# Kernel tuning notes

Measured on AMD Instinct MI355X. Metric: run time of the kernel, lower is better.

## Reference

```python
import jax, jax.numpy as jnp
import numpy as np

N = 100000      # nodes
E = 1600000     # edges (avg degree 16)
IN = 128        # input_dim
HID = 32        # hidden_dim per head (layer 1)
HEADS = 2       # heads (layer 1)
OUT = 32        # output_dim (layer 2, heads=1)
NEG_SLOPE = 0.2 # PyG GATConv default leaky relu slope


def setup_inputs() -> dict:
    key = jax.random.key(0)
    ks = jax.random.split(key, 10)
    s = 0.1  # glorot-ish scale
    x = jax.random.normal(ks[0], (N, IN), jnp.float32)
    edge_index = jax.random.randint(ks[1], (2, E), 0, N, dtype=jnp.int64)
    W1 = jax.random.normal(ks[2], (IN, HEADS * HID), jnp.float32) * s
    a1_src = jax.random.normal(ks[3], (HEADS, HID), jnp.float32) * s
    a1_dst = jax.random.normal(ks[4], (HEADS, HID), jnp.float32) * s
    b1 = jnp.zeros((HEADS * HID,), jnp.float32)
    W2 = jax.random.normal(ks[5], (HEADS * HID, OUT), jnp.float32) * s
    a2_src = jax.random.normal(ks[6], (1, OUT), jnp.float32) * s
    a2_dst = jax.random.normal(ks[7], (1, OUT), jnp.float32) * s
    b2 = jnp.zeros((OUT,), jnp.float32)
    return {"x": x, "edge_index": edge_index, "W1": W1, "a1_src": a1_src,
            "a1_dst": a1_dst, "b1": b1, "W2": W2, "a2_src": a2_src,
            "a2_dst": a2_dst, "b2": b2}


def _gat_layer(x, src, dst, W, a_src, a_dst, b, heads, out_ch, concat, n_nodes):
    # linear projection: [N, heads, out_ch]
    h = (x @ W).reshape(n_nodes, heads, out_ch)
    # per-node attention halves: [N, heads]
    alpha_s = jnp.einsum('nhc,hc->nh', h, a_src)
    alpha_d = jnp.einsum('nhc,hc->nh', h, a_dst)
    # per-edge raw score (message x_j = source node, softmax over dst segment)
    e = jax.nn.leaky_relu(alpha_s[src] + alpha_d[dst], NEG_SLOPE)  # [E, heads]
    # segment softmax over incoming edges of each dst node
    m = jax.ops.segment_max(e, dst, num_segments=n_nodes)          # [N, heads]
    m = jax.lax.stop_gradient(m)
    ee = jnp.exp(e - m[dst])
    denom = jax.ops.segment_sum(ee, dst, num_segments=n_nodes)     # [N, heads]
    alpha = ee / (denom[dst] + 1e-16)                              # [E, heads]
    # weighted scatter-add aggregation
    msg = h[src] * alpha[:, :, None]                               # [E, heads, out_ch]
    out = jax.ops.segment_sum(msg, dst, num_segments=n_nodes)      # [N, heads, out_ch]
    if concat:
        out = out.reshape(n_nodes, heads * out_ch)
    else:
        out = out.mean(axis=1)
    return out + b


def reference(x, edge_index, W1, a1_src, a1_dst, b1, W2, a2_src, a2_dst, b2):
    n = x.shape[0]
    # PyG GATConv adds self-loops by default (both layers, same edge set)
    loop = jnp.arange(n, dtype=edge_index.dtype)
    src = jnp.concatenate([edge_index[0], loop])
    dst = jnp.concatenate([edge_index[1], loop])
    h = _gat_layer(x, src, dst, W1, a1_src, a1_dst, b1, HEADS, HID, True, n)
    h = jax.nn.elu(h)
    return _gat_layer(h, src, dst, W2, a2_src, a2_dst, b2, 1, OUT, False, n)
```

## Files before the change

kernel.cpp:

```cpp
#include <hip/hip_runtime.h>
#include <math.h>

#define N_NODES 100000
#define N_EDGES 1600000
#define IN_DIM  128
#define C1      64
#define OUT_DIM 32
#define NEG_SLOPE 0.2f
#define LOG2E 1.44269504f

#define BSHIFT  8
#define BNODES  256
#define NBUCK   ((N_NODES + BNODES - 1) / BNODES)
#define CAP     5120
#define SLOTS   48
#define GC_STRIDE 16
#define G1_BLOCKS ((N_NODES + 127) / 128)

typedef _Float16 half8 __attribute__((ext_vector_type(8)));
typedef float    f32x4 __attribute__((ext_vector_type(4)));

__device__ __forceinline__ float wexp2(float sc) {
    return __builtin_amdgcn_exp2f(fmaxf(sc, NEG_SLOPE * sc));
}


__global__ void zero_k(int4* __restrict__ p, int n4) {
    int i = blockIdx.x * 256 + threadIdx.x;
    if (i < n4) p[i] = make_int4(0, 0, 0, 0);
}

__global__ __launch_bounds__(1024) void binp1_k(const int* __restrict__ ei,
        int* __restrict__ gcur, int* __restrict__ buf) {
    __shared__ int scnt[NBUCK], sbase[NBUCK], soff[NBUCK];
    int t = threadIdx.x;
    if (t < NBUCK) { scnt[t] = 0; soff[t] = 0; }
    __syncthreads();
    int  s[16], bk[16], ld[16];
    bool v[16];
    #pragma unroll
    for (int i = 0; i < 16; ++i) {
        int e = blockIdx.x * 16384 + i * 1024 + t;
        v[i] = e < N_EDGES;
        int ec = v[i] ? e : 0;
        s[i] = ei[ec];
        int d = ei[N_EDGES + ec];
        bk[i] = d >> BSHIFT;
        ld[i] = d & (BNODES - 1);
        if (v[i]) atomicAdd(&scnt[bk[i]], 1);
    }
    __syncthreads();
    if (t < NBUCK) sbase[t] = atomicAdd(&gcur[t * GC_STRIDE], scnt[t]);
    __syncthreads();
    #pragma unroll
    for (int i = 0; i < 16; ++i) {
        if (v[i]) {
            int p = sbase[bk[i]] + atomicAdd(&soff[bk[i]], 1);
            if (p < CAP) buf[bk[i] * CAP + p] = s[i] | (ld[i] << 17);
        }
    }
}

__global__ __launch_bounds__(256) void binp2_k(const int* __restrict__ gcur,
        const int* __restrict__ buf, int* __restrict__ csr, int* __restrict__ deg) {
    __shared__ int4 lcsr4[BNODES * SLOTS / 4];
    __shared__ int  lcnt[BNODES];
    int* lcsr = (int*)lcsr4;
    int b = blockIdx.x, t = threadIdx.x;
    lcnt[t] = 0;
    __syncthreads();
    int cnt = gcur[b * GC_STRIDE];
    if (cnt > CAP) cnt = CAP;
    const int* bb = buf + b * CAP;
    for (int e = t; e < cnt; e += 256) {
        int vv = bb[e];
        int src = vv & 0x1FFFF;
        int l = vv >> 17;
        int slot = atomicAdd(&lcnt[l], 1);
        if (slot < SLOTS) lcsr[l * SLOTS + slot] = src;
    }
    __syncthreads();
    int c = lcnt[t];
    int slot = c < SLOTS ? c : SLOTS - 1;
    lcsr[t * SLOTS + slot] = b * BNODES + t;
    int cd = c + 1;
    deg[b * BNODES + t] = cd < SLOTS ? cd : SLOTS;
    __syncthreads();
    int4* g4 = (int4*)csr + (size_t)b * (BNODES * SLOTS / 4);
    #pragma unroll
    for (int i = 0; i < BNODES * SLOTS / 4 / 256; ++i)
        g4[t + i * 256] = lcsr4[t + i * 256];
}

__global__ void prep_k(const float* __restrict__ W1, const float* __restrict__ W2,
                       _Float16* __restrict__ w1t, _Float16* __restrict__ w2t) {
    int t = blockIdx.x * 256 + threadIdx.x;
    if (t < IN_DIM * C1) {
        int k = t >> 6, n = t & 63;
        w1t[n * IN_DIM + k] = (_Float16)W1[t];
    }
    if (t < C1 * OUT_DIM) {
        int k = t >> 5, n = t & 31;
        w2t[n * C1 + k] = (_Float16)W2[t];
    }
}

__global__ __launch_bounds__(256) void gemm1_k(const float* __restrict__ x,
        const _Float16* __restrict__ w1t, const float* __restrict__ a_s,
        const float* __restrict__ a_d, _Float16* __restrict__ h,
        float* __restrict__ as_o, float* __restrict__ ad_o) {
    __shared__ _Float16 sh[4][32 * 72];
    int t = threadIdx.x;
    int wv = t >> 6, lane = t & 63, m = lane & 15, q = lane >> 4;
    int rbw = blockIdx.x * 128 + wv * 32;
    f32x4 acc[2][4];
    #pragma unroll
    for (int i = 0; i < 2; ++i)
        #pragma unroll
        for (int j = 0; j < 4; ++j) acc[i][j] = (f32x4){0.f, 0.f, 0.f, 0.f};
    #pragma unroll
    for (int ks = 0; ks < 4; ++ks) {
        half8 a[2];
        #pragma unroll
        for (int rt = 0; rt < 2; ++rt) {
            int r = rbw + rt * 16 + m;
            r = r < N_NODES ? r : 0;
            const float4* p = (const float4*)(x + (size_t)r * IN_DIM + ks * 32 + q * 8);
            float4 f0 = p[0], f1 = p[1];
            half8 av;
            av[0] = (_Float16)f0.x; av[1] = (_Float16)f0.y;
            av[2] = (_Float16)f0.z; av[3] = (_Float16)f0.w;
            av[4] = (_Float16)f1.x; av[5] = (_Float16)f1.y;
            av[6] = (_Float16)f1.z; av[7] = (_Float16)f1.w;
            a[rt] = av;
        }
        #pragma unroll
        for (int ct = 0; ct < 4; ++ct) {
            half8 b = *(const half8*)(w1t + (ct * 16 + m) * IN_DIM + ks * 32 + q * 8);
            acc[0][ct] = __builtin_amdgcn_mfma_f32_16x16x32_f16(a[0], b, acc[0][ct], 0, 0, 0);
            acc[1][ct] = __builtin_amdgcn_mfma_f32_16x16x32_f16(a[1], b, acc[1][ct], 0, 0, 0);
        }
    }
    _Float16* ws = sh[wv];
    #pragma unroll
    for (int rt = 0; rt < 2; ++rt)
        #pragma unroll
        for (int ct = 0; ct < 4; ++ct)
            #pragma unroll
            for (int r = 0; r < 4; ++r)
                ws[(rt * 16 + q * 4 + r) * 72 + ct * 16 + m] = (_Float16)acc[rt][ct][r];
    __syncthreads();
    int rl = lane >> 1, hp = lane & 1;
    int rg = rbw + rl;
    if (rg < N_NODES) {
        float As_r[32], Ad_r[32];
        const float4* ap = (const float4*)(a_s + hp * 32);
        const float4* dp = (const float4*)(a_d + hp * 32);
        #pragma unroll
        for (int i = 0; i < 8; ++i) {
            float4 v = ap[i];
            As_r[4*i] = v.x; As_r[4*i+1] = v.y; As_r[4*i+2] = v.z; As_r[4*i+3] = v.w;
            float4 u = dp[i];
            Ad_r[4*i] = u.x; Ad_r[4*i+1] = u.y; Ad_r[4*i+2] = u.z; Ad_r[4*i+3] = u.w;
        }
        const _Float16* rowp = ws + rl * 72 + hp * 32;
        half8 c0 = *(const half8*)(rowp);
        half8 c1 = *(const half8*)(rowp + 8);
        half8 c2 = *(const half8*)(rowp + 16);
        half8 c3 = *(const half8*)(rowp + 24);
        float s = 0.f, dd = 0.f;
        #pragma unroll
        for (int j = 0; j < 8; ++j) {
            s  = fmaf((float)c0[j], As_r[j],      s);
            dd = fmaf((float)c0[j], Ad_r[j],      dd);
            s  = fmaf((float)c1[j], As_r[8 + j],  s);
            dd = fmaf((float)c1[j], Ad_r[8 + j],  dd);
            s  = fmaf((float)c2[j], As_r[16 + j], s);
            dd = fmaf((float)c2[j], Ad_r[16 + j], dd);
            s  = fmaf((float)c3[j], As_r[24 + j], s);
            dd = fmaf((float)c3[j], Ad_r[24 + j], dd);
        }
        as_o[rg * 2 + hp] = s  * LOG2E;
        ad_o[rg * 2 + hp] = dd * LOG2E;
        _Float16* hr = h + (size_t)rg * C1 + hp * 32;
        *(half8*)(hr)      = c0;
        *(half8*)(hr + 8)  = c1;
        *(half8*)(hr + 16) = c2;
        *(half8*)(hr + 24) = c3;
    }
}

__global__ __launch_bounds__(256) void agg1g2_k(const int* __restrict__ deg,
        const int* __restrict__ csr, const _Float16* __restrict__ h1,
        const float* __restrict__ as1, const float* __restrict__ ad1,
        const float* __restrict__ b1, const _Float16* __restrict__ w2t,
        const float* __restrict__ a2s, const float* __restrict__ a2d,
        _Float16* __restrict__ h2, float* __restrict__ as2o,
        float* __restrict__ ad2o) {
    __shared__ _Float16 shu[16 * 72];
    __shared__ _Float16 sh2[16 * 36];
    int t = threadIdx.x;
    int wv = t >> 6, lane = t & 63;
    int dl   = lane >> 4;
    int eg   = (lane >> 3) & 1;
    int cl   = lane & 7;
    int head = cl >> 2;
    int lr   = wv * 4 + dl;
    int d    = blockIdx.x * 16 + lr;

    int cnt = deg[d];
    const int* row = csr + d * SLOTS;
    float advl = ad1[d * 2 + head];
    float acc[8] = {0.f, 0.f, 0.f, 0.f, 0.f, 0.f, 0.f, 0.f};
    float wsum = 0.f;
    for (int base = 0; base < cnt; base += 8) {
        int e0 = base + eg, e1 = e0 + 2, e2 = e0 + 4, e3 = e0 + 6;
        bool v0 = e0 < cnt, v1 = e1 < cnt, v2 = e2 < cnt, v3 = e3 < cnt;
        int s0 = row[v0 ? e0 : 0];
        int s1 = row[v1 ? e1 : 0];
        int s2 = row[v2 ? e2 : 0];
        int s3 = row[v3 ? e3 : 0];
        float a0 = as1[(unsigned)(s0 * 2 + head)];
        float a1 = as1[(unsigned)(s1 * 2 + head)];
        float a2 = as1[(unsigned)(s2 * 2 + head)];
        float a3 = as1[(unsigned)(s3 * 2 + head)];
        half8 g0 = *(const half8*)(h1 + (unsigned)(s0 * C1 + 8 * cl));
        half8 g1 = *(const half8*)(h1 + (unsigned)(s1 * C1 + 8 * cl));
        half8 g2 = *(const half8*)(h1 + (unsigned)(s2 * C1 + 8 * cl));
        half8 g3 = *(const half8*)(h1 + (unsigned)(s3 * C1 + 8 * cl));
        float w0 = v0 ? wexp2(a0 + advl) : 0.f;
        float w1 = v1 ? wexp2(a1 + advl) : 0.f;
        float w2 = v2 ? wexp2(a2 + advl) : 0.f;
        float w3 = v3 ? wexp2(a3 + advl) : 0.f;
        #pragma unroll
        for (int i = 0; i < 8; ++i) {
            acc[i] = fmaf((float)g0[i], w0, acc[i]);
            acc[i] = fmaf((float)g1[i], w1, acc[i]);
            acc[i] = fmaf((float)g2[i], w2, acc[i]);
            acc[i] = fmaf((float)g3[i], w3, acc[i]);
        }
        wsum += (w0 + w1) + (w2 + w3);
    }
    #pragma unroll
    for (int i = 0; i < 8; ++i) acc[i] += __shfl_xor(acc[i], 8);
    wsum += __shfl_xor(wsum, 8);
    if (eg == 0) {
        float inv = 1.f / (wsum + 1e-16f);
        const float4* bv = (const float4*)(b1 + 8 * cl);
        float o[8];
        #pragma unroll
        for (int i = 0; i < 4; ++i) {
            o[i]     = acc[i]     * inv + (&bv[0].x)[i];
            o[4 + i] = acc[4 + i] * inv + (&bv[1].x)[i];
        }
        half8 hv;
        #pragma unroll
        for (int i = 0; i < 8; ++i) {
            float e = o[i] > 0.f ? o[i] : __expf(o[i]) - 1.f;
            hv[i] = (_Float16)e;
        }
        *(half8*)(shu + lr * 72 + cl * 8) = hv;
    }
    __syncthreads();
    if (wv != 0) return;

    {
        int m = lane & 15, q = lane >> 4;
        f32x4 c2[2];
        c2[0] = (f32x4){0.f, 0.f, 0.f, 0.f};
        c2[1] = (f32x4){0.f, 0.f, 0.f, 0.f};
        #pragma unroll
        for (int ks = 0; ks < 2; ++ks) {
            half8 a = *(const half8*)(shu + m * 72 + ks * 32 + q * 8);
            #pragma unroll
            for (int ct = 0; ct < 2; ++ct) {
                half8 b = *(const half8*)(w2t + (ct * 16 + m) * C1 + ks * 32 + q * 8);
                c2[ct] = __builtin_amdgcn_mfma_f32_16x16x32_f16(a, b, c2[ct], 0, 0, 0);
            }
        }
        #pragma unroll
        for (int ct = 0; ct < 2; ++ct)
            #pragma unroll
            for (int r = 0; r < 4; ++r)
                sh2[(q * 4 + r) * 36 + ct * 16 + m] = (_Float16)c2[ct][r];
    }
    asm volatile("s_waitcnt lgkmcnt(0)" ::: "memory");

    {
        int r = lane & 15, p = lane >> 4;
        int rg = blockIdx.x * 16 + r;
        const float4* ap = (const float4*)(a2s + p * 8);
        const float4* dp = (const float4*)(a2d + p * 8);
        float4 av0 = ap[0], av1 = ap[1];
        float4 dv0 = dp[0], dv1 = dp[1];
        float As[8] = {av0.x, av0.y, av0.z, av0.w, av1.x, av1.y, av1.z, av1.w};
        float Ad[8] = {dv0.x, dv0.y, dv0.z, dv0.w, dv1.x, dv1.y, dv1.z, dv1.w};
        half8 c = *(const half8*)(sh2 + r * 36 + p * 8);
        float s = 0.f, dd = 0.f;
        #pragma unroll
        for (int j = 0; j < 8; ++j) {
            s  = fmaf((float)c[j], As[j], s);
            dd = fmaf((float)c[j], Ad[j], dd);
        }
        s  += __shfl_xor(s, 16);  s  += __shfl_xor(s, 32);
        dd += __shfl_xor(dd, 16); dd += __shfl_xor(dd, 32);
        if (p == 0) {
            as2o[rg] = s  * LOG2E;
            ad2o[rg] = dd * LOG2E;
        }
        *(half8*)(h2 + (size_t)rg * OUT_DIM + p * 8) = c;
    }
}

__global__ __launch_bounds__(256) void agg2_k(const int* __restrict__ deg,
        const int* __restrict__ csr, const _Float16* __restrict__ h2,
        const float* __restrict__ as2, const float* __restrict__ ad2,
        const float* __restrict__ b2, float* __restrict__ out) {
    int lane = threadIdx.x & 63;
    int dl   = lane >> 3;
    int eg   = (lane >> 2) & 1;
    int cl   = lane & 3;
    int d = ((blockIdx.x * 256 + threadIdx.x) >> 6) * 8 + dl;
    int cnt = deg[d];
    const int* row = csr + d * SLOTS;
    float advl = ad2[d];
    float acc[8] = {0.f, 0.f, 0.f, 0.f, 0.f, 0.f, 0.f, 0.f};
    float wsum = 0.f;
    for (int base = 0; base < cnt; base += 8) {
        int e0 = base + eg, e1 = e0 + 2, e2 = e0 + 4, e3 = e0 + 6;
        bool v0 = e0 < cnt, v1 = e1 < cnt, v2 = e2 < cnt, v3 = e3 < cnt;
        int s0 = row[v0 ? e0 : 0];
        int s1 = row[v1 ? e1 : 0];
        int s2 = row[v2 ? e2 : 0];
        int s3 = row[v3 ? e3 : 0];
        float a0 = as2[(unsigned)s0];
        float a1 = as2[(unsigned)s1];
        float a2 = as2[(unsigned)s2];
        float a3 = as2[(unsigned)s3];
        half8 g0 = *(const half8*)(h2 + (unsigned)(s0 * OUT_DIM + 8 * cl));
        half8 g1 = *(const half8*)(h2 + (unsigned)(s1 * OUT_DIM + 8 * cl));
        half8 g2 = *(const half8*)(h2 + (unsigned)(s2 * OUT_DIM + 8 * cl));
        half8 g3 = *(const half8*)(h2 + (unsigned)(s3 * OUT_DIM + 8 * cl));
        float w0 = v0 ? wexp2(a0 + advl) : 0.f;
        float w1 = v1 ? wexp2(a1 + advl) : 0.f;
        float w2 = v2 ? wexp2(a2 + advl) : 0.f;
        float w3 = v3 ? wexp2(a3 + advl) : 0.f;
        #pragma unroll
        for (int i = 0; i < 8; ++i) {
            acc[i] = fmaf((float)g0[i], w0, acc[i]);
            acc[i] = fmaf((float)g1[i], w1, acc[i]);
            acc[i] = fmaf((float)g2[i], w2, acc[i]);
            acc[i] = fmaf((float)g3[i], w3, acc[i]);
        }
        wsum += (w0 + w1) + (w2 + w3);
    }
    #pragma unroll
    for (int i = 0; i < 8; ++i) acc[i] += __shfl_xor(acc[i], 4);
    wsum += __shfl_xor(wsum, 4);
    if (eg == 0) {
        float inv = 1.f / (wsum + 1e-16f);
        const float4* bv = (const float4*)(b2 + 8 * cl);
        float4 o0, o1;
        o0.x = acc[0] * inv + bv[0].x; o0.y = acc[1] * inv + bv[0].y;
        o0.z = acc[2] * inv + bv[0].z; o0.w = acc[3] * inv + bv[0].w;
        o1.x = acc[4] * inv + bv[1].x; o1.y = acc[5] * inv + bv[1].y;
        o1.z = acc[6] * inv + bv[1].z; o1.w = acc[7] * inv + bv[1].w;
        float4* ow = (float4*)(out + (size_t)d * OUT_DIM + 8 * cl);
        ow[0] = o0;
        ow[1] = o1;
    }
}


extern "C" void kernel_launch(void* const* d_in, const int* in_sizes, int n_in,
                              void* d_out, int out_size, void* d_ws, size_t ws_size,
                              hipStream_t stream) {
    const float* x   = (const float*)d_in[0];
    const int*   ei  = (const int*)d_in[1];
    const float* W1  = (const float*)d_in[2];
    const float* a1s = (const float*)d_in[3];
    const float* a1d = (const float*)d_in[4];
    const float* b1  = (const float*)d_in[5];
    const float* W2  = (const float*)d_in[6];
    const float* a2s = (const float*)d_in[7];
    const float* a2d = (const float*)d_in[8];
    const float* b2  = (const float*)d_in[9];
    float* out = (float*)d_out;

    char* ws = (char*)d_ws;
    size_t off = 0;
    auto alloc = [&](size_t bytes) -> void* {
        void* p = ws + off;
        off = (off + bytes + 255) & ~(size_t)255;
        return p;
    };
    int* gcur      = (int*)alloc((size_t)NBUCK * GC_STRIDE * 4);
    int* buf       = (int*)alloc((size_t)NBUCK * CAP * 4);
    int* csr       = (int*)alloc((size_t)NBUCK * BNODES * SLOTS * 4);
    int* deg       = (int*)alloc((size_t)NBUCK * BNODES * 4);
    _Float16* w1t  = (_Float16*)alloc((size_t)IN_DIM * C1 * 2);
    _Float16* w2t  = (_Float16*)alloc((size_t)C1 * OUT_DIM * 2);
    _Float16* h1   = (_Float16*)alloc((size_t)N_NODES * C1 * 2);
    float* as1     = (float*)alloc((size_t)N_NODES * 2 * 4);
    float* ad1     = (float*)alloc((size_t)N_NODES * 2 * 4);
    _Float16* h2   = (_Float16*)alloc((size_t)N_NODES * OUT_DIM * 2);
    float* as2     = (float*)alloc((size_t)N_NODES * 4);
    float* ad2     = (float*)alloc((size_t)N_NODES * 4);

    const int ZN4 = NBUCK * GC_STRIDE / 4;
    zero_k<<<(ZN4 + 255) / 256, 256, 0, stream>>>((int4*)gcur, ZN4);
    binp1_k<<<(N_EDGES + 16383) / 16384, 1024, 0, stream>>>(ei, gcur, buf);
    binp2_k<<<NBUCK, 256, 0, stream>>>(gcur, buf, csr, deg);
    prep_k<<<(IN_DIM * C1 + 255) / 256, 256, 0, stream>>>(W1, W2, w1t, w2t);

    gemm1_k<<<G1_BLOCKS, 256, 0, stream>>>(x, w1t, a1s, a1d, h1, as1, ad1);
    agg1g2_k<<<N_NODES / 16, 256, 0, stream>>>(deg, csr, h1, as1, ad1, b1,
                                               w2t, a2s, a2d, h2, as2, ad2);
    agg2_k<<<N_NODES / 32, 256, 0, stream>>>(deg, csr, h2, as2, ad2, b2, out);
}
```

Before: 217.6 us.

## Fold gcur zeroing into prep, shrink binning blocks, stage CSR rows in LDS

The zeroing of the bucket counters moves into prep_k, which now runs before binning, so one kernel launch goes away. binp1 switches from 1024-thread to 256-thread blocks with four times as many blocks, and skips global atomics for buckets with a zero count. Both aggregation kernels load their block's CSR rows into shared memory with coalesced int4 reads, instead of each lane reading neighbour indices from global memory. A sched_barrier is added after the LDS wait in agg1g2. This costs more shared memory per block plus one extra __syncthreads, and binning now issues more global atomics because there are more blocks.

```diff
diff --git a/kernel.cpp b/kernel.cpp
--- a/kernel.cpp
+++ b/kernel.cpp
@@ -25,22 +25,17 @@
 }
 
 
-__global__ void zero_k(int4* __restrict__ p, int n4) {
-    int i = blockIdx.x * 256 + threadIdx.x;
-    if (i < n4) p[i] = make_int4(0, 0, 0, 0);
-}
-
-__global__ __launch_bounds__(1024) void binp1_k(const int* __restrict__ ei,
+__global__ __launch_bounds__(256) void binp1_k(const int* __restrict__ ei,
         int* __restrict__ gcur, int* __restrict__ buf) {
     __shared__ int scnt[NBUCK], sbase[NBUCK], soff[NBUCK];
     int t = threadIdx.x;
-    if (t < NBUCK) { scnt[t] = 0; soff[t] = 0; }
+    for (int i = t; i < NBUCK; i += 256) { scnt[i] = 0; soff[i] = 0; }
     __syncthreads();
     int  s[16], bk[16], ld[16];
     bool v[16];
     #pragma unroll
     for (int i = 0; i < 16; ++i) {
-        int e = blockIdx.x * 16384 + i * 1024 + t;
+        int e = blockIdx.x * 4096 + i * 256 + t;
         v[i] = e < N_EDGES;
         int ec = v[i] ? e : 0;
         s[i] = ei[ec];
@@ -50,7 +45,8 @@
         if (v[i]) atomicAdd(&scnt[bk[i]], 1);
     }
     __syncthreads();
-    if (t < NBUCK) sbase[t] = atomicAdd(&gcur[t * GC_STRIDE], scnt[t]);
+    for (int i = t; i < NBUCK; i += 256)
+        sbase[i] = scnt[i] ? atomicAdd(&gcur[i * GC_STRIDE], scnt[i]) : 0;
     __syncthreads();
     #pragma unroll
     for (int i = 0; i < 16; ++i) {
@@ -93,8 +89,10 @@
 }
 
 __global__ void prep_k(const float* __restrict__ W1, const float* __restrict__ W2,
-                       _Float16* __restrict__ w1t, _Float16* __restrict__ w2t) {
+                       _Float16* __restrict__ w1t, _Float16* __restrict__ w2t,
+                       int* __restrict__ gcur) {
     int t = blockIdx.x * 256 + threadIdx.x;
+    if (t < NBUCK * GC_STRIDE) gcur[t] = 0;
     if (t < IN_DIM * C1) {
         int k = t >> 6, n = t & 63;
         w1t[n * IN_DIM + k] = (_Float16)W1[t];
@@ -197,6 +195,7 @@
         const float* __restrict__ a2s, const float* __restrict__ a2d,
         _Float16* __restrict__ h2, float* __restrict__ as2o,
         float* __restrict__ ad2o) {
+    __shared__ int      srow[16 * SLOTS];
     __shared__ _Float16 shu[16 * 72];
     __shared__ _Float16 sh2[16 * 36];
     int t = threadIdx.x;
@@ -208,8 +207,12 @@
     int lr   = wv * 4 + dl;
     int d    = blockIdx.x * 16 + lr;
 
+    if (t < 16 * SLOTS / 4)
+        ((int4*)srow)[t] = ((const int4*)(csr + (size_t)blockIdx.x * 16 * SLOTS))[t];
+    __syncthreads();
+
     int cnt = deg[d];
-    const int* row = csr + d * SLOTS;
+    const int* row = srow + lr * SLOTS;
     float advl = ad1[d * 2 + head];
     float acc[8] = {0.f, 0.f, 0.f, 0.f, 0.f, 0.f, 0.f, 0.f};
     float wsum = 0.f;
@@ -285,6 +288,7 @@
                 sh2[(q * 4 + r) * 36 + ct * 16 + m] = (_Float16)c2[ct][r];
     }
     asm volatile("s_waitcnt lgkmcnt(0)" ::: "memory");
+    __builtin_amdgcn_sched_barrier(0);
 
     {
         int r = lane & 15, p = lane >> 4;
@@ -316,13 +320,25 @@
         const int* __restrict__ csr, const _Float16* __restrict__ h2,
         const float* __restrict__ as2, const float* __restrict__ ad2,
         const float* __restrict__ b2, float* __restrict__ out) {
-    int lane = threadIdx.x & 63;
+    __shared__ int srow[32 * SLOTS];
+    int t = threadIdx.x;
+    int wv = t >> 6, lane = t & 63;
     int dl   = lane >> 3;
     int eg   = (lane >> 2) & 1;
     int cl   = lane & 3;
-    int d = ((blockIdx.x * 256 + threadIdx.x) >> 6) * 8 + dl;
+    int lr   = wv * 8 + dl;
+    int d    = blockIdx.x * 32 + lr;
+
+    {
+        int4* s4 = (int4*)srow;
+        const int4* g4 = (const int4*)(csr + (size_t)blockIdx.x * 32 * SLOTS);
+        s4[t] = g4[t];
+        if (t < 128) s4[256 + t] = g4[256 + t];
+    }
+    __syncthreads();
+
     int cnt = deg[d];
-    const int* row = csr + d * SLOTS;
+    const int* row = srow + lr * SLOTS;
     float advl = ad2[d];
     float acc[8] = {0.f, 0.f, 0.f, 0.f, 0.f, 0.f, 0.f, 0.f};
     float wsum = 0.f;
@@ -407,11 +423,9 @@
     float* as2     = (float*)alloc((size_t)N_NODES * 4);
     float* ad2     = (float*)alloc((size_t)N_NODES * 4);
 
-    const int ZN4 = NBUCK * GC_STRIDE / 4;
-    zero_k<<<(ZN4 + 255) / 256, 256, 0, stream>>>((int4*)gcur, ZN4);
-    binp1_k<<<(N_EDGES + 16383) / 16384, 1024, 0, stream>>>(ei, gcur, buf);
+    prep_k<<<(IN_DIM * C1 + 255) / 256, 256, 0, stream>>>(W1, W2, w1t, w2t, gcur);
+    binp1_k<<<(N_EDGES + 4095) / 4096, 256, 0, stream>>>(ei, gcur, buf);
     binp2_k<<<NBUCK, 256, 0, stream>>>(gcur, buf, csr, deg);
-    prep_k<<<(IN_DIM * C1 + 255) / 256, 256, 0, stream>>>(W1, W2, w1t, w2t);
 
     gemm1_k<<<G1_BLOCKS, 256, 0, stream>>>(x, w1t, a1s, a1d, h1, as1, ad1);
     agg1g2_k<<<N_NODES / 16, 256, 0, stream>>>(deg, csr, h1, as1, ad1, b1,
```

New measurement: 216.7 us. Within noise of the previous version (-0.4%).
